# Performance work log

Hardware: AMD Instinct MI355X
Metric: run time of the kernel (lower is better)

Reference implementation:

```python
import jax, jax.numpy as jnp
import numpy as np

N = 50000      # movie nodes
E = 1000000    # edges per metapath
F_IN = 512
HID = 128
HEADS = 8
D = HID // HEADS  # 16
OUT = 3
NEG_SLOPE = 0.2   # PyG HANConv leaky_relu slope


def setup_inputs() -> dict:
    key = jax.random.key(0)
    ks = jax.random.split(key, 16)
    x = jax.random.normal(ks[0], (N, F_IN), jnp.float32)
    ei0 = jax.random.randint(ks[1], (2, E), 0, N, jnp.int32)
    ei1 = jax.random.randint(ks[2], (2, E), 0, N, jnp.int32)
    W_proj = jax.random.normal(ks[3], (F_IN, HID), jnp.float32) / np.sqrt(F_IN)
    b_proj = jnp.zeros((HID,), jnp.float32)
    att_src0 = jax.random.normal(ks[4], (HEADS, D), jnp.float32) / np.sqrt(D)
    att_dst0 = jax.random.normal(ks[5], (HEADS, D), jnp.float32) / np.sqrt(D)
    att_src1 = jax.random.normal(ks[6], (HEADS, D), jnp.float32) / np.sqrt(D)
    att_dst1 = jax.random.normal(ks[7], (HEADS, D), jnp.float32) / np.sqrt(D)
    Wk = jax.random.normal(ks[8], (HID, HID), jnp.float32) / np.sqrt(HID)
    bk = jnp.zeros((HID,), jnp.float32)
    q = jax.random.normal(ks[9], (HID,), jnp.float32) / np.sqrt(HID)
    W_lin = jax.random.normal(ks[10], (HID, OUT), jnp.float32) / np.sqrt(HID)
    b_lin = jnp.zeros((OUT,), jnp.float32)
    return dict(x=x, edge_index_mp0=ei0, edge_index_mp1=ei1,
                W_proj=W_proj, b_proj=b_proj,
                att_src0=att_src0, att_dst0=att_dst0,
                att_src1=att_src1, att_dst1=att_dst1,
                Wk=Wk, bk=bk, q=q, W_lin=W_lin, b_lin=b_lin)


def _han_edge_type(xp, src, dst, att_src, att_dst):
    """Node-level multi-head attention for one metapath (eval mode, no dropout).
    xp: [N, H, D] projected features; src/dst: [E] indices.
    """
    a_src = jnp.einsum('nhd,hd->nh', xp, att_src)  # [N, H]
    a_dst = jnp.einsum('nhd,hd->nh', xp, att_dst)
    alpha = jax.nn.leaky_relu(a_src[src] + a_dst[dst], NEG_SLOPE)  # [E, H]
    # segment softmax over incoming edges of each dst node
    amax = jax.ops.segment_max(alpha, dst, num_segments=N)
    amax = jnp.where(jnp.isfinite(amax), amax, 0.0)
    ex = jnp.exp(alpha - amax[dst])
    denom = jax.ops.segment_sum(ex, dst, num_segments=N)
    w = ex / (denom[dst] + 1e-16)                 # [E, H]
    msg = w[:, :, None] * xp[src]                 # [E, H, D]
    out = jax.ops.segment_sum(msg, dst, num_segments=N)  # [N, H, D]
    return jax.nn.relu(out.reshape(N, HID))


def reference(x, edge_index_mp0, edge_index_mp1, W_proj, b_proj,
              att_src0, att_dst0, att_src1, att_dst1,
              Wk, bk, q, W_lin, b_lin):
    xp = (x @ W_proj + b_proj).reshape(N, HEADS, D)
    o0 = _han_edge_type(xp, edge_index_mp0[0], edge_index_mp0[1], att_src0, att_dst0)
    o1 = _han_edge_type(xp, edge_index_mp1[0], edge_index_mp1[1], att_src1, att_dst1)
    outs = jnp.stack([o0, o1], axis=0)            # [M=2, N, HID]
    # semantic-level attention: score_m = sum(q * mean_n tanh(k_lin(o_m)))
    scores = jnp.einsum('mh,h->m', jnp.tanh(outs @ Wk + bk).mean(axis=1), q)
    beta = jax.nn.softmax(scores)                 # [2]
    fused = jnp.einsum('m,mnh->nh', beta, outs)   # [N, HID]
    return fused @ W_lin + b_lin                  # [N, OUT]
```

## Files before the change

kernel.cpp:

```cpp
#include <hip/hip_runtime.h>
#include <hip/hip_bf16.h>

#define NN 50000
#define EE 1000000
#define FIN 512
#define HIDDEN 128
#define NH 8
#define DH 16
#define NOUT 3
#define NBUCK 196
#define EPB 8192
#define NBLKA ((EE + EPB - 1) / EPB)
#define ATTBLK ((NN*NH + 255) / 256)

typedef unsigned short u16;
typedef unsigned int u32;
typedef __attribute__((ext_vector_type(8))) short short8;
typedef __attribute__((ext_vector_type(4))) float f32x4;

__device__ __forceinline__ float b2f(u16 b) { return __uint_as_float(((u32)b) << 16); }
__device__ __forceinline__ u16 f2b(float f) { return (u16)(__float_as_uint(f) >> 16); }
__device__ __forceinline__ u16 f2b_rne(float f) {
    u32 u = __float_as_uint(f);
    return (u16)((u + 0x7FFFu + ((u >> 16) & 1u)) >> 16);
}

__device__ __forceinline__ void gload16(const u16* g, u16* l) {
    __builtin_amdgcn_global_load_lds(
        (const __attribute__((address_space(1))) unsigned int*)(g),
        (__attribute__((address_space(3))) unsigned int*)(l), 16, 0, 0);
}

#define W_BP   65536
#define W_AS0  65664
#define W_BK   82560
#define W_Q    82688
#define W_WL   82816
#define W_BL   83200

__global__ __launch_bounds__(256) void k_prep(
    const void* __restrict__ x, const void* __restrict__ Wp, const void* __restrict__ Wk,
    const void* bp, const void* as0, const void* ad0, const void* as1, const void* ad1,
    const void* bk, const void* q, const void* Wl, const void* bl,
    int* __restrict__ flag, float* __restrict__ scores, int* __restrict__ curA,
    float* __restrict__ wconv, u16* __restrict__ WhiT, u16* __restrict__ WloT,
    u16* __restrict__ WkThi)
{
    const int t = threadIdx.x;
    const int bid = blockIdx.x;

    const u16* xb = (const u16*)x;
    {
        float v = b2f(xb[((t*16 + (bid & 15))*131)*2]);
        float a = fabsf(v);
        int insane = ((a == 0.0f) || (a >= 1e-8f && a <= 1e4f)) ? 0 : 1;
        __shared__ int red[256];
        red[t] = insane;
        __syncthreads();
        for (int s = 128; s > 0; s >>= 1) { if (t < s) red[t] += red[t+s]; __syncthreads(); }
        const int f = (red[0] > 64) ? 1 : 0;
        if (bid == 0 && t == 0) { flag[0] = f; scores[0] = 0.f; scores[1] = 0.f; }

        if (bid < 256) {
            int idx = bid*256 + t;
            float w = f ? ((const float*)Wp)[idx] : b2f(((const u16*)Wp)[idx]);
            int k = idx >> 7, n = idx & 127;
            u32 hb = __float_as_uint(w) & 0xFFFF0000u;
            WhiT[(size_t)n*FIN + k] = (u16)(hb >> 16);
            WloT[(size_t)n*FIN + k] = f2b(w - __uint_as_float(hb));
        } else if (bid < 320) {
            int i = (bid-256)*256 + t;
            float w = f ? ((const float*)Wk)[i] : b2f(((const u16*)Wk)[i]);
            int k = i >> 7, h = i & 127;
            WkThi[(size_t)h*HIDDEN + k] = f2b_rne(w);
        } else if (bid == 320) {
            #pragma unroll
            for (int j = 0; j < 6; ++j) {
                int i = j*256 + t;
                if (i < 1283) {
                    const void* src; int off; int dst;
                    if (i < 640) {
                        dst = W_BP + i;
                        if (i < 128)      { src = bp;  off = i; }
                        else if (i < 256) { src = as0; off = i-128; }
                        else if (i < 384) { src = ad0; off = i-256; }
                        else if (i < 512) { src = as1; off = i-384; }
                        else              { src = ad1; off = i-512; }
                    } else if (i < 896) {
                        dst = W_BK + (i-640);
                        if (i < 768) { src = bk; off = i-640; }
                        else         { src = q;  off = i-768; }
                    } else {
                        dst = W_WL + (i-896);
                        if (i < 1280) { src = Wl; off = i-896; }
                        else          { src = bl; off = i-1280; }
                    }
                    wconv[dst] = f ? ((const float*)src)[off] : b2f(((const u16*)src)[off]);
                }
            }
        } else {
            int i = (bid-321)*256 + t;
            if (i < 8192) curA[i] = 0;
        }
    }
}

__global__ __launch_bounds__(256) void k_projm(
    const void* __restrict__ xv, const u16* __restrict__ WhiT,
    const u16* __restrict__ WloT, const float* __restrict__ bpf,
    const int* __restrict__ flag, u16* __restrict__ xpb)
{
    __shared__ u16 lds[2][16384];
    const int t = threadIdx.x;
    const int lane = t & 63;
    const int wid = t >> 6;
    const int m16 = lane & 15;
    const int quad = lane >> 4;
    const int wr = wid >> 1, wc = wid & 1;
    const int blockRow = blockIdx.x * 128;

    f32x4 acc[4][4];
    #pragma unroll
    for (int i = 0; i < 4; ++i)
        #pragma unroll
        for (int j = 0; j < 4; ++j) acc[i][j] = (f32x4)(0.f);

    if (flag[0]) {
        const float* xf = (const float*)xv;
        const int srow = t >> 1;
        const int shalf = t & 1;
        int gxrow = blockRow + srow; if (gxrow >= NN) gxrow = NN - 1;
        const float* xr = xf + (size_t)gxrow * FIN + shalf * 16;
        const int ssw = (srow >> 1) & 3;
        const int aw0 = srow*32 + ((shalf*2)     ^ ssw) * 8;
        const int aw1 = srow*32 + ((shalf*2 + 1) ^ ssw) * 8;

        int bp0 = t, bp1 = t + 256;
        int br0 = bp0 >> 2, br1 = bp1 >> 2;
        int bc0 = (bp0 & 3) ^ ((br0 >> 1) & 3);
        int bc1 = (bp1 & 3) ^ ((br1 >> 1) & 3);
        const u16* srcBh0 = WhiT + (size_t)br0 * FIN + bc0 * 8;
        const u16* srcBh1 = WhiT + (size_t)br1 * FIN + bc1 * 8;
        const u16* srcBl0 = WloT + (size_t)br0 * FIN + bc0 * 8;
        const u16* srcBl1 = WloT + (size_t)br1 * FIN + bc1 * 8;
        const int dB0 = bp0 * 8, dB1 = bp1 * 8;

        int aoff[4], boff[4];
        #pragma unroll
        for (int mt = 0; mt < 4; ++mt) {
            int r = wr*64 + mt*16 + m16;
            aoff[mt] = r*32 + ((quad ^ ((r >> 1) & 3)) << 3);
        }
        #pragma unroll
        for (int nt = 0; nt < 4; ++nt) {
            int r = wc*64 + nt*16 + m16;
            boff[nt] = r*32 + ((quad ^ ((r >> 1) & 3)) << 3);
        }

        u16* Lc = lds[0];
        u16* Ln = lds[1];
        {
            float4 v0 = *(const float4*)(xr);
            float4 v1 = *(const float4*)(xr + 4);
            float4 v2 = *(const float4*)(xr + 8);
            float4 v3 = *(const float4*)(xr + 12);
            gload16(srcBh0, Lc + 8192  + dB0);
            gload16(srcBh1, Lc + 8192  + dB1);
            gload16(srcBl0, Lc + 12288 + dB0);
            gload16(srcBl1, Lc + 12288 + dB1);
            float xs[16] = {v0.x,v0.y,v0.z,v0.w, v1.x,v1.y,v1.z,v1.w,
                            v2.x,v2.y,v2.z,v2.w, v3.x,v3.y,v3.z,v3.w};
            short8 h0, h1, l0, l1;
            #pragma unroll
            for (int j = 0; j < 8; ++j) {
                u32 u = __float_as_uint(xs[j]);   u32 hb = u & 0xFFFF0000u;
                h0[j] = (short)(hb >> 16); l0[j] = (short)f2b(xs[j] - __uint_as_float(hb));
                u32 u2 = __float_as_uint(xs[8+j]); u32 hb2 = u2 & 0xFFFF0000u;
                h1[j] = (short)(hb2 >> 16); l1[j] = (short)f2b(xs[8+j] - __uint_as_float(hb2));
            }
            *(short8*)(Lc + aw0) = h0;
            *(short8*)(Lc + aw1) = h1;
            *(short8*)(Lc + 4096 + aw0) = l0;
            *(short8*)(Lc + 4096 + aw1) = l1;
        }
        __syncthreads();

        #pragma unroll 1
        for (int ks = 0; ks < 16; ++ks) {
            const int kt = (ks + 1) * 32;
            float4 v0, v1, v2, v3;
            if (ks < 15) {
                v0 = *(const float4*)(xr + kt);
                v1 = *(const float4*)(xr + kt + 4);
                v2 = *(const float4*)(xr + kt + 8);
                v3 = *(const float4*)(xr + kt + 12);
                gload16(srcBh0 + kt, Ln + 8192  + dB0);
                gload16(srcBh1 + kt, Ln + 8192  + dB1);
                gload16(srcBl0 + kt, Ln + 12288 + dB0);
                gload16(srcBl1 + kt, Ln + 12288 + dB1);
            }
            short8 bh[4], bl[4];
            #pragma unroll
            for (int nt = 0; nt < 4; ++nt) {
                bh[nt] = *(const short8*)(Lc + 8192  + boff[nt]);
                bl[nt] = *(const short8*)(Lc + 12288 + boff[nt]);
            }
            #pragma unroll
            for (int mt = 0; mt < 4; ++mt) {
                short8 ah = *(const short8*)(Lc + aoff[mt]);
                short8 al = *(const short8*)(Lc + 4096 + aoff[mt]);
                #pragma unroll
                for (int nt = 0; nt < 4; ++nt) {
                    acc[mt][nt] = __builtin_amdgcn_mfma_f32_16x16x32_bf16(ah, bh[nt], acc[mt][nt], 0,0,0);
                    acc[mt][nt] = __builtin_amdgcn_mfma_f32_16x16x32_bf16(ah, bl[nt], acc[mt][nt], 0,0,0);
                    acc[mt][nt] = __builtin_amdgcn_mfma_f32_16x16x32_bf16(al, bh[nt], acc[mt][nt], 0,0,0);
                }
            }
            if (ks < 15) {
                float xs[16] = {v0.x,v0.y,v0.z,v0.w, v1.x,v1.y,v1.z,v1.w,
                                v2.x,v2.y,v2.z,v2.w, v3.x,v3.y,v3.z,v3.w};
                short8 h0, h1, l0, l1;
                #pragma unroll
                for (int j = 0; j < 8; ++j) {
                    u32 u = __float_as_uint(xs[j]);   u32 hb = u & 0xFFFF0000u;
                    h0[j] = (short)(hb >> 16); l0[j] = (short)f2b(xs[j] - __uint_as_float(hb));
                    u32 u2 = __float_as_uint(xs[8+j]); u32 hb2 = u2 & 0xFFFF0000u;
                    h1[j] = (short)(hb2 >> 16); l1[j] = (short)f2b(xs[8+j] - __uint_as_float(hb2));
                }
                *(short8*)(Ln + aw0) = h0;
                *(short8*)(Ln + aw1) = h1;
                *(short8*)(Ln + 4096 + aw0) = l0;
                *(short8*)(Ln + 4096 + aw1) = l1;
            }
            __syncthreads();
            u16* tmp = Lc; Lc = Ln; Ln = tmp;
        }
    } else {
        const u16* xb = (const u16*)xv;
        const int r0 = t >> 2,         c0 = (t & 3) * 8;
        const int r1 = (t + 256) >> 2, c1 = ((t + 256) & 3) * 8;
        int g0 = blockRow + r0; if (g0 >= NN) g0 = NN - 1;
        int g1 = blockRow + r1; if (g1 >= NN) g1 = NN - 1;
        const u16* srcA0  = xb   + (size_t)g0 * FIN + c0;
        const u16* srcA1  = xb   + (size_t)g1 * FIN + c1;
        const u16* srcBh0 = WhiT + (size_t)r0 * FIN + c0;
        const u16* srcBh1 = WhiT + (size_t)r1 * FIN + c1;
        const u16* srcBl0 = WloT + (size_t)r0 * FIN + c0;
        const u16* srcBl1 = WloT + (size_t)r1 * FIN + c1;

#define PSTAGE(buf, kt) do { \
        gload16(srcA0  + (kt), &lds[buf][t*8]); \
        gload16(srcA1  + (kt), &lds[buf][2048 + t*8]); \
        gload16(srcBh0 + (kt), &lds[buf][4096 + t*8]); \
        gload16(srcBh1 + (kt), &lds[buf][6144 + t*8]); \
        gload16(srcBl0 + (kt), &lds[buf][8192 + t*8]); \
        gload16(srcBl1 + (kt), &lds[buf][10240 + t*8]); \
    } while (0)

        PSTAGE(0, 0);
        __syncthreads();
        int cur = 0;
        for (int ks = 0; ks < 16; ++ks) {
            if (ks < 15) {
                if (cur) PSTAGE(0, (ks + 1) * 32);
                else     PSTAGE(1, (ks + 1) * 32);
            }
            const u16* L = lds[cur];
            short8 a[4], bh[4], bl[4];
            #pragma unroll
            for (int mt = 0; mt < 4; ++mt)
                a[mt] = *(const short8*)&L[(wr*64 + mt*16 + m16)*32 + quad*8];
            #pragma unroll
            for (int nt = 0; nt < 4; ++nt) {
                bh[nt] = *(const short8*)&L[4096 + (wc*64 + nt*16 + m16)*32 + quad*8];
                bl[nt] = *(const short8*)&L[8192 + (wc*64 + nt*16 + m16)*32 + quad*8];
            }
            #pragma unroll
            for (int mt = 0; mt < 4; ++mt)
                #pragma unroll
                for (int nt = 0; nt < 4; ++nt) {
                    acc[mt][nt] = __builtin_amdgcn_mfma_f32_16x16x32_bf16(a[mt], bh[nt], acc[mt][nt], 0,0,0);
                    acc[mt][nt] = __builtin_amdgcn_mfma_f32_16x16x32_bf16(a[mt], bl[nt], acc[mt][nt], 0,0,0);
                }
            __syncthreads();
            cur ^= 1;
        }
#undef PSTAGE
    }

    #pragma unroll
    for (int nt = 0; nt < 4; ++nt) {
        int col = wc*64 + nt*16 + m16;
        float bias = bpf[col];
        #pragma unroll
        for (int mt = 0; mt < 4; ++mt) {
            int orow0 = blockRow + wr*64 + mt*16 + quad*4;
            #pragma unroll
            for (int r = 0; r < 4; ++r) {
                int orow = orow0 + r;
                if (orow < NN) xpb[(size_t)orow*HIDDEN + col] = f2b_rne(acc[mt][nt][r] + bias);
            }
        }
    }
}

__global__ __launch_bounds__(256) void k_fused1(
    const u16* __restrict__ xpb, const float* __restrict__ watt,
    float* __restrict__ o_as0, float* __restrict__ o_ad0,
    float* __restrict__ o_as1, float* __restrict__ o_ad1,
    const int* __restrict__ ei0, const int* __restrict__ ei1,
    int* __restrict__ curA, u32* __restrict__ tmp0, u32* __restrict__ tmp1)
{
    __shared__ int sh[768];
    const int t = threadIdx.x;
    const int bid = blockIdx.x;

    if (bid < ATTBLK) {
        float* s0 = (float*)sh;
        float* d0 = s0 + 128;
        float* s1 = s0 + 256;
        float* d1 = s0 + 384;
        if (t < 128) { s0[t]=watt[t]; d0[t]=watt[128+t]; s1[t]=watt[256+t]; d1[t]=watt[384+t]; }
        __syncthreads();
        int tid = bid*256 + t;
        if (tid >= NN*NH) return;
        int h = tid & 7;
        const u32* px = (const u32*)(xpb + (size_t)tid * DH);
        float xv[16];
        #pragma unroll
        for (int i=0;i<8;++i){ u32 v=px[i]; xv[i*2]=b2f((u16)(v&0xFFFF)); xv[i*2+1]=b2f((u16)(v>>16)); }
        float r0=0.f,r1=0.f,r2=0.f,r3=0.f;
        #pragma unroll
        for (int d=0; d<16; ++d) {
            float xvd = xv[d];
            r0 += xvd*s0[h*16+d]; r1 += xvd*d0[h*16+d];
            r2 += xvd*s1[h*16+d]; r3 += xvd*d1[h*16+d];
        }
        o_as0[tid]=r0; o_ad0[tid]=r1; o_as1[tid]=r2; o_ad1[tid]=r3;
    } else {
        int r = bid - ATTBLK;
        const int mp = (r >= NBLKA) ? 1 : 0;
        const int bx = r - mp*NBLKA;
        const int* ei = mp ? ei1 : ei0;
        u32* tmp = mp ? tmp1 : tmp0;
        int* hist = sh;
        int* seg  = sh + 256;
        int* cnt  = sh + 512;
        for (int b = t; b < NBUCK; b += 256) hist[b] = 0;
        __syncthreads();
        const int e0 = bx * EPB;
        #pragma unroll
        for (int i = 0; i < EPB/256; ++i) {
            int idx = e0 + i*256 + t;
            if (idx < EE) atomicAdd(&hist[ei[EE + idx] >> 8], 1);
        }
        __syncthreads();
        for (int b = t; b < NBUCK; b += 256) {
            int h = hist[b];
            seg[b] = h ? atomicAdd(&curA[(mp*256 + b)*16], h) : 0;
            cnt[b] = 0;
        }
        __syncthreads();
        #pragma unroll
        for (int i = 0; i < EPB/256; ++i) {
            int idx = e0 + i*256 + t;
            if (idx < EE) {
                int s = ei[idx], d = ei[EE + idx];
                int b = d >> 8;
                int pos = seg[b] + atomicAdd(&cnt[b], 1);
                tmp[((size_t)b << 13) + pos] = (u32)(((d & 255) << 16) | s);
            }
        }
    }
}

__global__ __launch_bounds__(256) void k_scatterB(
    const u32* __restrict__ tmp0, const u32* __restrict__ tmp1,
    const int* __restrict__ bcap,
    int* __restrict__ ns0, int* __restrict__ ns1,
    int* __restrict__ nc0, int* __restrict__ nc1,
    int* __restrict__ srt0, int* __restrict__ srt1)
{
    const int b = blockIdx.x;
    const int mp = blockIdx.y;
    const u32* tmp = mp ? tmp1 : tmp0;
    int* nstart = mp ? ns1 : ns0;
    int* ncnt   = mp ? nc1 : nc0;
    int* srt    = mp ? srt1 : srt0;
    const int cntb = bcap[(mp*256 + b)*16];
    const int segbase = b << 13;
    __shared__ int lcnt[256];
    __shared__ int loff[256];
    const int t = threadIdx.x;
    lcnt[t] = 0;
    __syncthreads();
    for (int i = t; i < cntb; i += 256)
        atomicAdd(&lcnt[tmp[segbase + i] >> 16], 1);
    __syncthreads();
    int v = lcnt[t];
    loff[t] = v;
    __syncthreads();
    for (int off = 1; off < 256; off <<= 1) {
        int u = (t >= off) ? loff[t - off] : 0;
        __syncthreads();
        loff[t] += u;
        __syncthreads();
    }
    int excl = loff[t] - v;
    int node = (b << 8) + t;
    if (node < NN) { nstart[node] = segbase + excl; ncnt[node] = v; }
    __syncthreads();
    loff[t] = excl;
    lcnt[t] = 0;
    __syncthreads();
    for (int i = t; i < cntb; i += 256) {
        u32 p = tmp[segbase + i];
        int local = p >> 16;
        int pos = segbase + loff[local] + atomicAdd(&lcnt[local], 1);
        srt[pos] = (int)(p & 0xFFFFu);
    }
}

__global__ __launch_bounds__(256) void k_gather(
    const int* __restrict__ srt0, const int* __restrict__ srt1,
    const int* __restrict__ ns0, const int* __restrict__ ns1,
    const int* __restrict__ nc0, const int* __restrict__ nc1,
    const float* __restrict__ as0, const float* __restrict__ ad0,
    const float* __restrict__ as1, const float* __restrict__ ad1,
    const u16* __restrict__ xpb, u16* __restrict__ obf0, u16* __restrict__ obf1)
{
    const int t = threadIdx.x;
    const int wid = blockIdx.x*4 + (t >> 6);
    if (wid >= NN) return;
    const int lane = t & 63;
    const int hc = lane & 7;
    const int eg = lane >> 3;
    const int mp = blockIdx.y;
    const int*  srt  = mp ? srt1  : srt0;
    const int*  nstart = mp ? ns1 : ns0;
    const int*  ncnt   = mp ? nc1 : nc0;
    const float* asr = mp ? as1 : as0;
    const float* ads = mp ? ad1 : ad0;
    u16* obf = mp ? obf1 : obf0;
    const u32* xw = (const u32*)xpb;

    const int b = nstart[wid], e = b + ncnt[wid];
    const float adv = ads[wid*NH + hc];
    const int bp = (lane >> 3) << 2;
    float accx = 0.f, accy = 0.f, den = 0.f;

    for (int i = b; i < e; i += 8) {
        int il = i + eg;
        int ilc = il < e ? il : e - 1;
        int s = srt[ilc];

        u32 rv0, rv1, rv2, rv3, rv4, rv5, rv6, rv7;
        {
            const u32* r0p = xw + ((size_t)(u32)__builtin_amdgcn_readlane(s, 0)  << 6);
            const u32* r1p = xw + ((size_t)(u32)__builtin_amdgcn_readlane(s, 8)  << 6);
            const u32* r2p = xw + ((size_t)(u32)__builtin_amdgcn_readlane(s, 16) << 6);
            const u32* r3p = xw + ((size_t)(u32)__builtin_amdgcn_readlane(s, 24) << 6);
            const u32* r4p = xw + ((size_t)(u32)__builtin_amdgcn_readlane(s, 32) << 6);
            const u32* r5p = xw + ((size_t)(u32)__builtin_amdgcn_readlane(s, 40) << 6);
            const u32* r6p = xw + ((size_t)(u32)__builtin_amdgcn_readlane(s, 48) << 6);
            const u32* r7p = xw + ((size_t)(u32)__builtin_amdgcn_readlane(s, 56) << 6);
            rv0 = r0p[lane]; rv1 = r1p[lane]; rv2 = r2p[lane]; rv3 = r3p[lane];
            rv4 = r4p[lane]; rv5 = r5p[lane]; rv6 = r6p[lane]; rv7 = r7p[lane];
        }

        float av = asr[s*NH + hc] + adv;
        av = fmaxf(av, 0.2f*av);
        float w = (il < e) ? __expf(av) : 0.f;
        int wi = __float_as_int(w);

        #pragma unroll
        for (int k2 = 0; k2 < 8; ++k2) {
            float wk = __int_as_float(__builtin_amdgcn_ds_bpermute(bp + k2*32, wi));
            u32 v = (k2==0)?rv0:(k2==1)?rv1:(k2==2)?rv2:(k2==3)?rv3:
                    (k2==4)?rv4:(k2==5)?rv5:(k2==6)?rv6:rv7;
            accx = fmaf(wk, b2f((u16)(v & 0xFFFF)), accx);
            accy = fmaf(wk, b2f((u16)(v >> 16)), accy);
            den += wk;
        }
    }
    float inv = 1.f / (den + 1e-16f);
    u32 lo = f2b_rne(accx*inv), hi = f2b_rne(accy*inv);
    ((u32*)obf)[(size_t)wid*64 + lane] = (hi << 16) | lo;
}

__global__ __launch_bounds__(256) void k_semantic(
    const u16* __restrict__ obf0, const u16* __restrict__ obf1,
    const u16* __restrict__ WkThi, const float* __restrict__ bkf,
    const float* __restrict__ qf, float* __restrict__ scores)
{
    const int t = threadIdx.x;
    const int lane = t & 63;
    const int w = t >> 6;
    const int m16 = lane & 15;
    const int quad = lane >> 4;
    const int mp = blockIdx.y;
    const u16* om = mp ? obf1 : obf0;
    const int tile = blockIdx.x*4 + w;

    float partial = 0.f;
    if (tile < NN/16) {
        int row = tile*16 + m16;
        f32x4 acc[8];
        #pragma unroll
        for (int i=0;i<8;++i) acc[i] = (f32x4)(0.f);

        for (int kt = 0; kt < HIDDEN; kt += 32) {
            int kbase = kt + quad*8;
            short8 a = *(const short8*)(om + (size_t)row*HIDDEN + kbase);
            #pragma unroll
            for (int j=0;j<8;++j) a[j] = ((u16)a[j] & 0x8000u) ? (short)0 : a[j];
            #pragma unroll
            for (int nt = 0; nt < 8; ++nt) {
                int n = nt*16 + m16;
                short8 bhi = *(const short8*)(WkThi + (size_t)n*HIDDEN + kbase);
                acc[nt] = __builtin_amdgcn_mfma_f32_16x16x32_bf16(a, bhi, acc[nt], 0,0,0);
            }
        }
        #pragma unroll
        for (int nt=0; nt<8; ++nt) {
            int col = nt*16 + m16;
            float bkv = bkf[col], qv = qf[col];
            #pragma unroll
            for (int r=0;r<4;++r) {
                float xx = acc[nt][r] + bkv;
                xx = fminf(fmaxf(xx, -10.f), 10.f);
                float tex = __expf(2.f*xx);
                partial += qv * ((tex - 1.f) / (tex + 1.f));
            }
        }
    }
    __shared__ float red[256];
    red[t] = partial;
    __syncthreads();
    for (int s2 = 128; s2 > 0; s2 >>= 1) {
        if (t < s2) red[t] += red[t + s2];
        __syncthreads();
    }
    if (t == 0) unsafeAtomicAdd(&scores[mp], red[0]);
}

__global__ __launch_bounds__(256) void k_final(
    const u16* __restrict__ obf0, const u16* __restrict__ obf1,
    const float* __restrict__ scores, const float* __restrict__ Wlf,
    const float* __restrict__ blf, const int* __restrict__ flag,
    void* __restrict__ outv)
{
    __shared__ float fus[16*128];
    __shared__ float WlL[384];
    __shared__ float blL[3];
    const int t = threadIdx.x;
    for (int i = t; i < 384; i += 256) WlL[i] = Wlf[i];
    if (t < 3) blL[t] = blf[t];
    float sc0 = scores[0] / (float)NN;
    float sc1 = scores[1] / (float)NN;
    float m = fmaxf(sc0, sc1);
    float e0 = __expf(sc0-m), e1 = __expf(sc1-m);
    float binv = 1.f/(e0+e1);
    float b0 = e0*binv, b1 = e1*binv;

    const u32* o0w = (const u32*)obf0;
    const u32* o1w = (const u32*)obf1;
    size_t base = (size_t)blockIdx.x * 16 * 64;
    #pragma unroll
    for (int i=0;i<4;++i) {
        int j = t + i*256;
        u32 v0 = o0w[base + j];
        u32 v1 = o1w[base + j];
        float l0 = fmaxf(b2f((u16)(v0&0xFFFF)),0.f), h0 = fmaxf(b2f((u16)(v0>>16)),0.f);
        float l1 = fmaxf(b2f((u16)(v1&0xFFFF)),0.f), h1 = fmaxf(b2f((u16)(v1>>16)),0.f);
        int row = j >> 6, cp = j & 63;
        fus[row*128 + cp*2]     = b0*l0 + b1*l1;
        fus[row*128 + cp*2 + 1] = b0*h0 + b1*h1;
    }
    __syncthreads();
    if (t < 48) {
        int node = t / 3, c = t % 3;
        float acc = blL[c];
        const float* fr = &fus[node*128];
        #pragma unroll 16
        for (int k=0;k<128;++k) acc += fr[k]*WlL[k*3+c];
        size_t oi = (size_t)(blockIdx.x*16 + node)*NOUT + c;
        if (flag[0]) ((float*)outv)[oi] = acc;
        else         ((__hip_bfloat16*)outv)[oi] = __float2bfloat16(acc);
    }
}

extern "C" void kernel_launch(void* const* d_in, const int* in_sizes, int n_in,
                              void* d_out, int out_size, void* d_ws, size_t ws_size,
                              hipStream_t stream)
{
    const void* x   = d_in[0];
    const int* ei0  = (const int*)d_in[1];
    const int* ei1  = (const int*)d_in[2];

    float* ws = (float*)d_ws;
    u16*   xpb     = (u16*)ws;
    float* a_src0  = ws +  3200000;
    float* a_dst0  = ws +  3600000;
    float* a_src1  = ws +  4000000;
    float* a_dst1  = ws +  4400000;
    u16*   obf0    = (u16*)(ws + 4800000);
    u16*   obf1    = (u16*)(ws + 8000000);
    int*   srt0    = (int*)(ws + 11200000);
    int*   srt1    = (int*)(ws + 12810000);
    u32*   tmp0    = (u32*)(ws + 14420000);
    u32*   tmp1    = (u32*)(ws + 16030000);
    int*   nstart0 = (int*)(ws + 17640000);
    int*   nstart1 = (int*)(ws + 17690000);
    int*   ncnt0   = (int*)(ws + 17740000);
    int*   ncnt1   = (int*)(ws + 17790000);
    float* scores  = ws + 17840000;
    int*   flag    = (int*)(ws + 17840004);
    float* wconv   = ws + 17840008;
    int*   curA    = (int*)(ws + 17923216);
    u16*   WhiT    = (u16*)(ws + 17931408);
    u16*   WloT    = (u16*)(ws + 17964176);
    u16*   WkThi   = (u16*)(ws + 17996944);

    k_prep<<<353, 256, 0, stream>>>(
        x, d_in[3], d_in[9], d_in[4], d_in[5], d_in[6], d_in[7], d_in[8],
        d_in[10], d_in[11], d_in[12], d_in[13],
        flag, scores, curA, wconv, WhiT, WloT, WkThi);

    k_projm<<<(NN+127)/128, 256, 0, stream>>>(x, WhiT, WloT, wconv + W_BP, flag, xpb);

    k_fused1<<<ATTBLK + 2*NBLKA, 256, 0, stream>>>(
        xpb, wconv + W_AS0, a_src0, a_dst0, a_src1, a_dst1,
        ei0, ei1, curA, tmp0, tmp1);

    k_scatterB<<<dim3(NBUCK,2), 256, 0, stream>>>(
        tmp0, tmp1, curA, nstart0, nstart1, ncnt0, ncnt1, srt0, srt1);

    k_gather<<<dim3((NN + 3)/4, 2), 256, 0, stream>>>(
        srt0, srt1, nstart0, nstart1, ncnt0, ncnt1,
        a_src0, a_dst0, a_src1, a_dst1, xpb, obf0, obf1);

    k_semantic<<<dim3((NN/16 + 3)/4, 2), 256, 0, stream>>>(
        obf0, obf1, WkThi, wconv + W_BK, wconv + W_Q, scores);

    k_final<<<NN/16, 256, 0, stream>>>(obf0, obf1, scores, wconv + W_WL, wconv + W_BL,
                                       flag, d_out);
}
```

Before: 406.0 us.

## Stage bucket scatter in LDS for coalesced writes and narrow sorted indices to u16

The edge bucketing kernel now computes per-bucket offsets with a block-wide prefix scan and packs edges into a shared-memory buffer first. Each wavefront then copies one contiguous bucket run to global memory, instead of every edge being written to a scattered address. The per-node counting sort in k_scatterB also stages into LDS and writes contiguously, and the sorted source index array is narrowed from int to u16 to halve its traffic in the gather. The cost is 32KB of static LDS in k_fused1, which also applies to the attention-score blocks and may reduce their occupancy.

```diff
diff --git a/kernel.cpp b/kernel.cpp
--- a/kernel.cpp
+++ b/kernel.cpp
@@ -311,15 +311,19 @@
     const int* __restrict__ ei0, const int* __restrict__ ei1,
     int* __restrict__ curA, u32* __restrict__ tmp0, u32* __restrict__ tmp1)
 {
-    __shared__ int sh[768];
+    __shared__ u32 ebuf[EPB];
+    __shared__ int shA[256];
+    __shared__ int shB[256];
+    __shared__ int shC[256];
+    __shared__ int shD[256];
     const int t = threadIdx.x;
     const int bid = blockIdx.x;
 
     if (bid < ATTBLK) {
-        float* s0 = (float*)sh;
+        float* s0 = (float*)shA;
         float* d0 = s0 + 128;
-        float* s1 = s0 + 256;
-        float* d1 = s0 + 384;
+        float* s1 = (float*)shB;
+        float* d1 = s1 + 128;
         if (t < 128) { s0[t]=watt[t]; d0[t]=watt[128+t]; s1[t]=watt[256+t]; d1[t]=watt[384+t]; }
         __syncthreads();
         int tid = bid*256 + t;
@@ -343,23 +347,30 @@
         const int bx = r - mp*NBLKA;
         const int* ei = mp ? ei1 : ei0;
         u32* tmp = mp ? tmp1 : tmp0;
-        int* hist = sh;
-        int* seg  = sh + 256;
-        int* cnt  = sh + 512;
-        for (int b = t; b < NBUCK; b += 256) hist[b] = 0;
-        __syncthreads();
         const int e0 = bx * EPB;
+        const int wid = t >> 6, lane = t & 63;
+
+        shA[t] = 0;
+        __syncthreads();
         #pragma unroll
         for (int i = 0; i < EPB/256; ++i) {
             int idx = e0 + i*256 + t;
-            if (idx < EE) atomicAdd(&hist[ei[EE + idx] >> 8], 1);
-        }
-        __syncthreads();
-        for (int b = t; b < NBUCK; b += 256) {
-            int h = hist[b];
-            seg[b] = h ? atomicAdd(&curA[(mp*256 + b)*16], h) : 0;
-            cnt[b] = 0;
-        }
+            if (idx < EE) atomicAdd(&shA[ei[EE + idx] >> 8], 1);
+        }
+        __syncthreads();
+        int v = shA[t];
+        shB[t] = v;
+        __syncthreads();
+        for (int off = 1; off < 256; off <<= 1) {
+            int u = (t >= off) ? shB[t - off] : 0;
+            __syncthreads();
+            shB[t] += u;
+            __syncthreads();
+        }
+        int excl = shB[t] - v;
+        shB[t] = excl;
+        shC[t] = 0;
+        shD[t] = (t < NBUCK && v) ? atomicAdd(&curA[(mp*256 + t)*16], v) : 0;
         __syncthreads();
         #pragma unroll
         for (int i = 0; i < EPB/256; ++i) {
@@ -367,9 +378,18 @@
             if (idx < EE) {
                 int s = ei[idx], d = ei[EE + idx];
                 int b = d >> 8;
-                int pos = seg[b] + atomicAdd(&cnt[b], 1);
-                tmp[((size_t)b << 13) + pos] = (u32)(((d & 255) << 16) | s);
-            }
+                int pos = shB[b] + atomicAdd(&shC[b], 1);
+                ebuf[pos] = (u32)(((d & 255) << 16) | s);
+            }
+        }
+        __syncthreads();
+        for (int b = wid; b < NBUCK; b += 4) {
+            int h = shA[b];
+            if (!h) continue;
+            int lb = shB[b];
+            u32 gb = ((u32)b << 13) + (u32)shD[b];
+            for (int k = lane; k < h; k += 64)
+                tmp[gb + k] = ebuf[lb + k];
         }
     }
 }
@@ -379,16 +399,17 @@
     const int* __restrict__ bcap,
     int* __restrict__ ns0, int* __restrict__ ns1,
     int* __restrict__ nc0, int* __restrict__ nc1,
-    int* __restrict__ srt0, int* __restrict__ srt1)
+    u16* __restrict__ srt0, u16* __restrict__ srt1)
 {
     const int b = blockIdx.x;
     const int mp = blockIdx.y;
     const u32* tmp = mp ? tmp1 : tmp0;
     int* nstart = mp ? ns1 : ns0;
     int* ncnt   = mp ? nc1 : nc0;
-    int* srt    = mp ? srt1 : srt0;
+    u16* srt    = mp ? srt1 : srt0;
     const int cntb = bcap[(mp*256 + b)*16];
     const int segbase = b << 13;
+    __shared__ u16 sl[EPB];
     __shared__ int lcnt[256];
     __shared__ int loff[256];
     const int t = threadIdx.x;
@@ -416,13 +437,16 @@
     for (int i = t; i < cntb; i += 256) {
         u32 p = tmp[segbase + i];
         int local = p >> 16;
-        int pos = segbase + loff[local] + atomicAdd(&lcnt[local], 1);
-        srt[pos] = (int)(p & 0xFFFFu);
-    }
+        int pos = loff[local] + atomicAdd(&lcnt[local], 1);
+        sl[pos] = (u16)(p & 0xFFFFu);
+    }
+    __syncthreads();
+    for (int i = t; i < cntb; i += 256)
+        srt[segbase + i] = sl[i];
 }
 
 __global__ __launch_bounds__(256) void k_gather(
-    const int* __restrict__ srt0, const int* __restrict__ srt1,
+    const u16* __restrict__ srt0, const u16* __restrict__ srt1,
     const int* __restrict__ ns0, const int* __restrict__ ns1,
     const int* __restrict__ nc0, const int* __restrict__ nc1,
     const float* __restrict__ as0, const float* __restrict__ ad0,
@@ -436,7 +460,7 @@
     const int hc = lane & 7;
     const int eg = lane >> 3;
     const int mp = blockIdx.y;
-    const int*  srt  = mp ? srt1  : srt0;
+    const u16*  srt  = mp ? srt1  : srt0;
     const int*  nstart = mp ? ns1 : ns0;
     const int*  ncnt   = mp ? nc1 : nc0;
     const float* asr = mp ? as1 : as0;
@@ -606,8 +630,8 @@
     float* a_dst1  = ws +  4400000;
     u16*   obf0    = (u16*)(ws + 4800000);
     u16*   obf1    = (u16*)(ws + 8000000);
-    int*   srt0    = (int*)(ws + 11200000);
-    int*   srt1    = (int*)(ws + 12810000);
+    u16*   srt0    = (u16*)(ws + 11200000);
+    u16*   srt1    = (u16*)(ws + 12810000);
     u32*   tmp0    = (u32*)(ws + 14420000);
     u32*   tmp1    = (u32*)(ws + 16030000);
     int*   nstart0 = (int*)(ws + 17640000);
```

Result: faster. 396.2 us (-2.4%).
